# Kernel optimization log

Measured on AMD Instinct MI355X. Metric: run time of the kernel, lower is better.

## Reference

```python
import jax, jax.numpy as jnp
import numpy as np

N, E, DIN, H, DOUT = 50000, 1600000, 16, 256, 2
EPS = 1e-5


def _glorot(key, shape):
    fan_in = shape[0]
    return jax.random.normal(key, shape, dtype=jnp.float32) * (1.0 / np.sqrt(fan_in))


def setup_inputs() -> dict:
    key = jax.random.key(0)
    ks = jax.random.split(key, 16)
    x = jax.random.normal(ks[0], (N, DIN), dtype=jnp.float32)
    edge_index = jax.random.randint(ks[1], (2, E), 0, N, dtype=jnp.int64)
    edge_weight = jax.random.uniform(ks[2], (E,), dtype=jnp.float32)
    return {
        "x": x,
        "edge_index": edge_index,
        "edge_weight": edge_weight,
        # GCN layer 1 and 2
        "W1": _glorot(ks[3], (DIN, H)), "b1": jnp.zeros((H,), jnp.float32),
        "g1": jnp.ones((H,), jnp.float32), "be1": jnp.zeros((H,), jnp.float32),
        "W2": _glorot(ks[4], (H, H)), "b2": jnp.zeros((H,), jnp.float32),
        "g2": jnp.ones((H,), jnp.float32), "be2": jnp.zeros((H,), jnp.float32),
        # GRU (single layer): weight_ih [3H, H], weight_hh [3H, H]
        "Wih": _glorot(ks[5], (H, 3 * H)).T * 0.5,
        "Whh": _glorot(ks[6], (H, 3 * H)).T * 0.5,
        "bih": jnp.zeros((3 * H,), jnp.float32),
        "bhh": jnp.zeros((3 * H,), jnp.float32),
        # decoder MLP
        "Wd1": _glorot(ks[7], (H + DIN, H)), "bd1": jnp.zeros((H,), jnp.float32),
        "Wd2": _glorot(ks[8], (H, H // 2)), "bd2": jnp.zeros((H // 2,), jnp.float32),
        "Wd3": _glorot(ks[9], (H // 2, DOUT)), "bd3": jnp.zeros((DOUT,), jnp.float32),
    }


def _gcn_conv(x, W, b, src, dst, ew, n):
    # GCNConv(improved=True): A_hat = A + 2I, sym-normalized, messages aggregated at dst
    xw = x @ W  # [n, H]
    sl = jnp.arange(n, dtype=src.dtype)
    src_f = jnp.concatenate([src, sl])
    dst_f = jnp.concatenate([dst, sl])
    ew_f = jnp.concatenate([ew, jnp.full((n,), 2.0, ew.dtype)])
    deg = jax.ops.segment_sum(ew_f, dst_f, num_segments=n)
    dis = jnp.where(deg > 0, jax.lax.rsqrt(jnp.maximum(deg, 1e-12)), 0.0)
    norm = dis[src_f] * ew_f * dis[dst_f]  # [E+n]
    out = jax.ops.segment_sum(xw[src_f] * norm[:, None], dst_f, num_segments=n)
    return out + b


def _layernorm(h, g, be):
    mu = jnp.mean(h, axis=-1, keepdims=True)
    var = jnp.mean(jnp.square(h - mu), axis=-1, keepdims=True)
    return (h - mu) * jax.lax.rsqrt(var + EPS) * g + be


def _gru_step(x, h, Wih, Whh, bih, bhh):
    gi = x @ Wih.T + bih  # [n, 3H]
    gh = h @ Whh.T + bhh
    i_r, i_z, i_n = jnp.split(gi, 3, axis=-1)
    h_r, h_z, h_n = jnp.split(gh, 3, axis=-1)
    r = jax.nn.sigmoid(i_r + h_r)
    z = jax.nn.sigmoid(i_z + h_z)
    n = jnp.tanh(i_n + r * h_n)
    return (1.0 - z) * n + z * h


def reference(x, edge_index, edge_weight, W1, b1, g1, be1, W2, b2, g2, be2,
              Wih, Whh, bih, bhh, Wd1, bd1, Wd2, bd2, Wd3, bd3):
    n = x.shape[0]
    src, dst = edge_index[0], edge_index[1]
    # spatial encoding (eval mode: dropout off)
    h = _gcn_conv(x, W1, b1, src, dst, edge_weight, n)
    h = jax.nn.relu(_layernorm(h, g1, be1))
    h = _gcn_conv(h, W2, b2, src, dst, edge_weight, n)
    h = _layernorm(h, g2, be2)  # last layer: no relu
    # GRU single timestep, zero initial hidden state per agent
    h0 = jnp.zeros_like(h)
    temporal = _gru_step(h, h0, Wih, Whh, bih, bhh)
    # decoder MLP on [temporal, x]
    d = jnp.concatenate([temporal, x], axis=-1)
    d = jax.nn.relu(d @ Wd1 + bd1)
    d = jax.nn.relu(d @ Wd2 + bd2)
    pred = d @ Wd3 + bd3
    return jnp.clip(pred, -5.0, 5.0)
```

## Files before the change

### kernel.cpp

```cpp
#include <hip/hip_runtime.h>
#include <math.h>

#define N_NODES 50000
#define N_EDGES 1600000
#define DIN 16
#define H 256
#define RPB 16
#define LN_EPS 1e-5f
#define FIXS 8388608.0f
#define NB 391
#define CAP 5120
#define TILEA 4096
#define NTILES 391
#define GRU_COLS 48
#define GRU_STR 272
#define DSTR 264

typedef __attribute__((ext_vector_type(8))) unsigned short u16x8;
typedef __attribute__((ext_vector_type(8))) __bf16 bf16x8;
typedef __attribute__((ext_vector_type(4))) float f32x4;

__device__ inline unsigned short f2bf(float f) {
    unsigned u = __builtin_bit_cast(unsigned, f);
    return (unsigned short)((u + 0x7FFFu + ((u >> 16) & 1u)) >> 16);
}
__device__ inline float bf2f(unsigned short u) {
    return __builtin_bit_cast(float, ((unsigned)u) << 16);
}
__device__ inline float fsig(float x) { return 1.0f / (1.0f + __expf(-x)); }
__device__ inline float ftanh(float x) { return 2.0f / (1.0f + __expf(-2.0f * x)) - 1.0f; }

__global__ void k_detect(const void* ei, int* flag) {
    const long long* p = (const long long*)ei;
    bool is64 = true;
    for (int i = 0; i < 8; ++i) {
        long long v = p[i];
        if (v < 0 || v >= N_NODES) is64 = false;
    }
    *flag = is64 ? 1 : 0;
}

__global__ void k_zeroi(int* p, int n) {
    int i = blockIdx.x * blockDim.x + threadIdx.x;
    if (i < n) p[i] = 0;
}

__global__ void k_wprep(const float* Wih, const float* W2, const float* Wd1, const float* Wd2,
                        const float* x, unsigned short* Wg, unsigned short* W2T,
                        unsigned short* Wd1T, unsigned short* Wd2T, unsigned short* din) {
    int idx = blockIdx.x * blockDim.x + threadIdx.x;
    if (idx < 768 * 256) { Wg[idx] = f2bf(Wih[idx]); return; }
    idx -= 768 * 256;
    if (idx < 256 * 256) { int k = idx >> 8, n = idx & 255; W2T[n * 256 + k] = f2bf(W2[idx]); return; }
    idx -= 256 * 256;
    if (idx < 256 * 288) {
        int n = idx / 288, k = idx % 288;
        Wd1T[idx] = (k < 272) ? f2bf(Wd1[k * 256 + n]) : (unsigned short)0;
        return;
    }
    idx -= 256 * 288;
    if (idx < 128 * 256) { int k = idx >> 7, n = idx & 127; Wd2T[n * 256 + k] = f2bf(Wd2[idx]); return; }
    idx -= 128 * 256;
    if (idx < N_NODES * 32) {
        int row = idx >> 5, j = idx & 31;
        din[(long long)row * 288 + 256 + j] = (j < 16) ? f2bf(x[row * DIN + j]) : (unsigned short)0;
    }
}

__global__ __launch_bounds__(256) void k_msplit(const void* ei, const int* flag, const float* ew,
                                                int* bcursor, unsigned long long* stage) {
    __shared__ int bh[512], bscn[512], cur[512], gbase[512];
    __shared__ int ws4[4];
    __shared__ unsigned long long sdata[TILEA];
    __shared__ unsigned short sbkt[TILEA];
    int t = threadIdx.x;
    long long base = (long long)blockIdx.x * TILEA;
    int nhere = (int)(((long long)N_EDGES - base) < TILEA ? (N_EDGES - base) : TILEA);
    for (int i = t; i < 512; i += 256) bh[i] = 0;
    __syncthreads();
    bool f64 = (*flag != 0);
    unsigned long long vreg[TILEA / 256];
    int breg[TILEA / 256];
#pragma unroll
    for (int k = 0; k < TILEA / 256; ++k) {
        long long e = base + k * 256 + t;
        if (e < N_EDGES) {
            int s, d;
            if (f64) {
                const long long* p = (const long long*)ei;
                s = (int)p[e]; d = (int)p[N_EDGES + e];
            } else {
                const int* p = (const int*)ei;
                s = p[e]; d = p[N_EDGES + e];
            }
            unsigned wbits = __builtin_bit_cast(unsigned, ew[e]);
            vreg[k] = ((unsigned long long)wbits << 32) |
                      ((unsigned long long)(d & 127) << 16) | (unsigned)(s & 0xFFFF);
            breg[k] = d >> 7;
            atomicAdd(&bh[breg[k]], 1);
        } else breg[k] = -1;
    }
    __syncthreads();
    int a0 = bh[2 * t], a1 = bh[2 * t + 1];
    int s = a0 + a1;
    int lane = t & 63, wv = t >> 6;
    int sc = s;
    for (int d = 1; d < 64; d <<= 1) { int u = __shfl_up(sc, d, 64); if (lane >= d) sc += u; }
    if (lane == 63) ws4[wv] = sc;
    __syncthreads();
    int wpre = 0;
    for (int i = 0; i < wv; ++i) wpre += ws4[i];
    int excl = wpre + sc - s;
    bscn[2 * t] = excl;      cur[2 * t] = excl;
    bscn[2 * t + 1] = excl + a0; cur[2 * t + 1] = excl + a0;
    __syncthreads();
    for (int i = t; i < NB; i += 256) {
        int c = bh[i];
        if (c) gbase[i] = atomicAdd(&bcursor[i], c);
    }
    __syncthreads();
#pragma unroll
    for (int k = 0; k < TILEA / 256; ++k) {
        if (breg[k] >= 0) {
            int p = atomicAdd(&cur[breg[k]], 1);
            sdata[p] = vreg[k];
            sbkt[p] = (unsigned short)breg[k];
        }
    }
    __syncthreads();
    for (int i = t; i < nhere; i += 256) {
        int b = sbkt[i];
        stage[(long long)b * CAP + gbase[b] + (i - bscn[b])] = sdata[i];
    }
}

__global__ __launch_bounds__(256) void k_bfin(const unsigned long long* __restrict__ stage,
                                              const int* __restrict__ bcursor,
                                              float* __restrict__ dis,
                                              int* __restrict__ offs, int* __restrict__ oend,
                                              unsigned* __restrict__ csr) {
    __shared__ unsigned long long acc[128];
    __shared__ int sc[128];
    __shared__ int cur[128];
    int b = blockIdx.x, t = threadIdx.x;
    if (t < 128) acc[t] = 0ULL;
    __syncthreads();
    long long e0 = (long long)b * CAP;
    int n = bcursor[b];
    for (int i = t; i < n; i += 256) {
        unsigned long long v = stage[e0 + i];
        int nl = (int)((v >> 16) & 127);
        float w = __builtin_bit_cast(float, (unsigned)(v >> 32));
        atomicAdd(&acc[nl], (1ULL << 43) | (unsigned long long)llrintf(w * FIXS));
    }
    __syncthreads();
    int mycnt = 0;
    if (t < 128) {
        unsigned long long v = acc[t];
        mycnt = (int)(v >> 43);
        sc[t] = mycnt;
        int node = (b << 7) + t;
        if (node < N_NODES)
            dis[node] = rsqrtf((float)(v & ((1ULL << 43) - 1)) * (1.0f / FIXS) + 2.0f);
    }
    __syncthreads();
    for (int d = 1; d < 128; d <<= 1) {
        int v = 0;
        if (t < 128 && t >= d) v = sc[t - d];
        __syncthreads();
        if (t < 128 && t >= d) sc[t] += v;
        __syncthreads();
    }
    if (t < 128) {
        int excl = sc[t] - mycnt;
        cur[t] = excl;
        int node = (b << 7) + t;
        if (node < N_NODES) {
            offs[node] = (int)(e0 + excl);
            oend[node] = (int)(e0 + excl + mycnt);
        }
    }
    __syncthreads();
    for (int i = t; i < n; i += 256) {
        unsigned long long v = stage[e0 + i];
        int nl = (int)((v >> 16) & 127);
        int p = atomicAdd(&cur[nl], 1);
        float w = __builtin_bit_cast(float, (unsigned)(v >> 32));
        csr[e0 + p] = ((unsigned)f2bf(w) << 16) | (unsigned)(v & 0xFFFFu);
    }
}

__global__ void k_xpb(const float* x, const float* dis, unsigned short* xpb) {
    int idx = blockIdx.x * blockDim.x + threadIdx.x;
    if (idx >= N_NODES * DIN) return;
    xpb[idx] = f2bf(dis[idx >> 4] * x[idx]);
}

__global__ __launch_bounds__(256) void k_l1(const unsigned short* __restrict__ xpb,
        const int* __restrict__ offs, const int* __restrict__ oend,
        const unsigned* __restrict__ csr, const float* __restrict__ dis,
        const float* __restrict__ W, const float* __restrict__ bias,
        const float* __restrict__ g, const float* __restrict__ be,
        unsigned short* __restrict__ out) {
    __shared__ float s[RPB][H + 1];
    __shared__ float smu[RPB], srs[RPB];
    int t = threadIdx.x;
    long long rowbase = (long long)blockIdx.x * RPB;
    {
        int r = blockIdx.x * 16 + (t >> 4);
        int dd = t & 15;
        float di = dis[r];
        float xself = bf2f(xpb[(long long)r * DIN + dd]);
        float acc = 0.0f;
        int e0 = offs[r], e1 = oend[r];
        for (int e = e0; e < e1; e += 8) {
            unsigned vv[8];
#pragma unroll
            for (int j = 0; j < 8; ++j) {
                int idx = e + j;
                vv[j] = (idx < e1) ? csr[idx] : (unsigned)r;
            }
            float xx[8];
#pragma unroll
            for (int j = 0; j < 8; ++j) {
                int sidx = (int)(vv[j] & 0xFFFFu);
                xx[j] = bf2f(xpb[(long long)sidx * DIN + dd]);
            }
#pragma unroll
            for (int j = 0; j < 8; ++j) {
                float c = bf2f((unsigned short)(vv[j] >> 16));
                acc = fmaf(c, xx[j], acc);
            }
        }
        s[t >> 4][dd] = di * acc + 2.0f * di * xself;
    }
    __syncthreads();
    float acc2[RPB];
    float bb0 = bias[t];
#pragma unroll
    for (int r = 0; r < RPB; ++r) acc2[r] = bb0;
    for (int k = 0; k < DIN; ++k) {
        float wv = W[k * H + t];
#pragma unroll
        for (int r = 0; r < RPB; ++r) acc2[r] = fmaf(s[r][k], wv, acc2[r]);
    }
    __syncthreads();
#pragma unroll
    for (int r = 0; r < RPB; ++r) s[r][t] = acc2[r];
    __syncthreads();
    int lane = t & 63, wv2 = t >> 6;
    for (int rr = wv2; rr < RPB; rr += 4) {
        float v0 = s[rr][lane], v1 = s[rr][lane + 64], v2 = s[rr][lane + 128], v3 = s[rr][lane + 192];
        float sm = v0 + v1 + v2 + v3;
        float sq = v0 * v0 + v1 * v1 + v2 * v2 + v3 * v3;
        for (int d = 32; d; d >>= 1) {
            sm += __shfl_down(sm, d, 64);
            sq += __shfl_down(sq, d, 64);
        }
        if (lane == 0) {
            float mu = sm * (1.0f / H);
            float var = sq * (1.0f / H) - mu * mu;
            smu[rr] = mu;
            srs[rr] = rsqrtf(var + LN_EPS);
        }
    }
    __syncthreads();
    float gg = g[t], bb = be[t];
#pragma unroll
    for (int r = 0; r < RPB; ++r) {
        float h = fmaxf((acc2[r] - smu[r]) * srs[r] * gg + bb, 0.0f);
        out[(rowbase + r) * H + t] = f2bf(h * dis[rowbase + r]);
    }
}

__global__ __launch_bounds__(256) void k_spmm(const unsigned short* __restrict__ hin,
                                              unsigned short* __restrict__ hout,
                                              const int* __restrict__ offs,
                                              const int* __restrict__ oend,
                                              const unsigned* __restrict__ csr,
                                              const float* __restrict__ dis) {
    int t = threadIdx.x;
    int wv = t >> 6, lane = t & 63;
    int row = blockIdx.x * 4 + wv;
    const ushort4* h4 = (const ushort4*)hin;
    float di = dis[row];
    ushort4 vs = h4[(long long)row * 64 + lane];
    float a0 = 0.f, a1 = 0.f, a2 = 0.f, a3 = 0.f;
    int e0 = offs[row], e1 = oend[row];
    for (int e = e0; e < e1; e += 16) {
        unsigned vv[16];
#pragma unroll
        for (int j = 0; j < 16; ++j) {
            int idx = e + j;
            vv[j] = (idx < e1) ? csr[idx] : (unsigned)row;
        }
        ushort4 uu[16];
#pragma unroll
        for (int j = 0; j < 16; ++j) {
            int s = (int)(vv[j] & 0xFFFFu);
            uu[j] = h4[(long long)s * 64 + lane];
        }
#pragma unroll
        for (int j = 0; j < 16; ++j) {
            float c = bf2f((unsigned short)(vv[j] >> 16));
            a0 = fmaf(c, bf2f(uu[j].x), a0);
            a1 = fmaf(c, bf2f(uu[j].y), a1);
            a2 = fmaf(c, bf2f(uu[j].z), a2);
            a3 = fmaf(c, bf2f(uu[j].w), a3);
        }
    }
    ushort4 o;
    o.x = f2bf(di * a0 + 2.0f * di * bf2f(vs.x));
    o.y = f2bf(di * a1 + 2.0f * di * bf2f(vs.y));
    o.z = f2bf(di * a2 + 2.0f * di * bf2f(vs.z));
    o.w = f2bf(di * a3 + 2.0f * di * bf2f(vs.w));
    ((ushort4*)hout)[(long long)row * 64 + lane] = o;
}


__global__ __launch_bounds__(256) void k_ln_mfma(const unsigned short* __restrict__ in,
        const unsigned short* __restrict__ WT, const float* __restrict__ bias,
        const float* __restrict__ g, const float* __restrict__ be,
        unsigned short* __restrict__ outbf) {
    int t = threadIdx.x;
    int wv = t >> 6, l = t & 63;
    int lr = l & 15, lg = l >> 4;
    int rb = blockIdx.x * 64 + wv * 16;
    int arow = rb + lr; if (arow >= N_NODES) arow = N_NODES - 1;
    bf16x8 af[8];
    const unsigned short* ap = in + (long long)arow * H + lg * 8;
#pragma unroll
    for (int ks = 0; ks < 8; ++ks) af[ks] = __builtin_bit_cast(bf16x8, *(const u16x8*)(ap + ks * 32));
    f32x4 acc[16];
#pragma unroll
    for (int ct = 0; ct < 16; ++ct) acc[ct] = (f32x4){0.f, 0.f, 0.f, 0.f};
    for (int ct = 0; ct < 16; ++ct) {
        const unsigned short* wr = WT + (ct * 16 + lr) * H + lg * 8;
#pragma unroll
        for (int ks = 0; ks < 8; ++ks) {
            bf16x8 bfv = __builtin_bit_cast(bf16x8, *(const u16x8*)(wr + ks * 32));
            acc[ct] = __builtin_amdgcn_mfma_f32_16x16x32_bf16(af[ks], bfv, acc[ct], 0, 0, 0);
        }
    }
#pragma unroll
    for (int ct = 0; ct < 16; ++ct) {
        float bb = bias[ct * 16 + lr];
#pragma unroll
        for (int q = 0; q < 4; ++q) acc[ct][q] += bb;
    }
    float mean[4], rstd[4];
#pragma unroll
    for (int q = 0; q < 4; ++q) {
        float s = 0.f, s2 = 0.f;
#pragma unroll
        for (int ct = 0; ct < 16; ++ct) { float v = acc[ct][q]; s += v; s2 += v * v; }
#pragma unroll
        for (int m = 1; m < 16; m <<= 1) { s += __shfl_xor(s, m, 64); s2 += __shfl_xor(s2, m, 64); }
        float mu = s * (1.0f / H);
        mean[q] = mu;
        rstd[q] = rsqrtf(s2 * (1.0f / H) - mu * mu + LN_EPS);
    }
#pragma unroll
    for (int ct = 0; ct < 16; ++ct) {
        int col = ct * 16 + lr;
        float gg = g[col], bb = be[col];
#pragma unroll
        for (int q = 0; q < 4; ++q) {
            int row = rb + lg * 4 + q;
            if (row < N_NODES) {
                float nv = (acc[ct][q] - mean[q]) * rstd[q] * gg + bb;
                outbf[(long long)row * H + col] = f2bf(nv);
            }
        }
    }
}

__global__ __launch_bounds__(256) void k_gru_lds(const unsigned short* __restrict__ h2,
        const unsigned short* __restrict__ Wg, const float* __restrict__ bih,
        const float* __restrict__ bhh, unsigned short* __restrict__ din) {
    __shared__ unsigned short wbuf[2][GRU_COLS * GRU_STR];
    int t = threadIdx.x;
    int wv = t >> 6, l = t & 63;
    int lr = l & 15, lg = l >> 4;
    int rb = blockIdx.x * 64 + wv * 16;
    int arow = rb + lr; if (arow >= N_NODES) arow = N_NODES - 1;
    bf16x8 af[8];
    const unsigned short* ap = h2 + (long long)arow * H + lg * 8;
#pragma unroll
    for (int ks = 0; ks < 8; ++ks) af[ks] = __builtin_bit_cast(bf16x8, *(const u16x8*)(ap + ks * 32));

    auto stage = [&](int ct, int b) {
#pragma unroll
        for (int j = 0; j < 6; ++j) {
            int i = t + j * 256;
            int col = i >> 5;
            int off = (i & 31) * 8;
            int gate = col >> 4, c = col & 15;
            u16x8 v = *(const u16x8*)(Wg + ((gate * 256 + ct * 16 + c) * 256 + off));
            *(u16x8*)(&wbuf[b][col * GRU_STR + off]) = v;
        }
    };
    stage(0, 0);
    __syncthreads();
    for (int ct = 0; ct < 16; ++ct) {
        if (ct < 15) stage(ct + 1, (ct + 1) & 1);
        const unsigned short* cur = wbuf[ct & 1];
        f32x4 aR = (f32x4){0.f, 0.f, 0.f, 0.f};
        f32x4 aZ = aR, aN = aR;
        const unsigned short* base = cur + lr * GRU_STR + lg * 8;
#pragma unroll
        for (int ks = 0; ks < 8; ++ks) {
            bf16x8 b0 = __builtin_bit_cast(bf16x8, *(const u16x8*)(base + ks * 32));
            bf16x8 b1 = __builtin_bit_cast(bf16x8, *(const u16x8*)(base + 16 * GRU_STR + ks * 32));
            bf16x8 b2 = __builtin_bit_cast(bf16x8, *(const u16x8*)(base + 32 * GRU_STR + ks * 32));
            aR = __builtin_amdgcn_mfma_f32_16x16x32_bf16(af[ks], b0, aR, 0, 0, 0);
            aZ = __builtin_amdgcn_mfma_f32_16x16x32_bf16(af[ks], b1, aZ, 0, 0, 0);
            aN = __builtin_amdgcn_mfma_f32_16x16x32_bf16(af[ks], b2, aN, 0, 0, 0);
        }
        int col = ct * 16 + lr;
        float bR = bih[col] + bhh[col];
        float bZ = bih[col + 256] + bhh[col + 256];
        float bN = bih[col + 512];
        float hN = bhh[col + 512];
#pragma unroll
        for (int q = 0; q < 4; ++q) {
            int row = rb + lg * 4 + q;
            float r = fsig(aR[q] + bR);
            float z = fsig(aZ[q] + bZ);
            float n = ftanh(aN[q] + bN + r * hN);
            if (row < N_NODES) din[(long long)row * 288 + col] = f2bf((1.0f - z) * n);
        }
        __syncthreads();
    }
}

__global__ __launch_bounds__(256) void k_dec(const unsigned short* __restrict__ din,
        const unsigned short* __restrict__ W1T, const float* __restrict__ b1d,
        const unsigned short* __restrict__ W2T, const float* __restrict__ bd2,
        const float* __restrict__ Wd3, const float* __restrict__ bd3, float* __restrict__ out) {
    __shared__ unsigned short dtile[64][DSTR];
    int t = threadIdx.x;
    int wv = t >> 6, l = t & 63;
    int lr = l & 15, lg = l >> 4;
    int rb = blockIdx.x * 64 + wv * 16;
    int arow = rb + lr; if (arow >= N_NODES) arow = N_NODES - 1;
    {
        bf16x8 af[9];
        const unsigned short* ap = din + (long long)arow * 288 + lg * 8;
#pragma unroll
        for (int ks = 0; ks < 9; ++ks) af[ks] = __builtin_bit_cast(bf16x8, *(const u16x8*)(ap + ks * 32));
        f32x4 acc[16];
#pragma unroll
        for (int ct = 0; ct < 16; ++ct) acc[ct] = (f32x4){0.f, 0.f, 0.f, 0.f};
        for (int ct = 0; ct < 16; ++ct) {
            const unsigned short* wr = W1T + (ct * 16 + lr) * 288 + lg * 8;
#pragma unroll
            for (int ks = 0; ks < 9; ++ks) {
                bf16x8 bfv = __builtin_bit_cast(bf16x8, *(const u16x8*)(wr + ks * 32));
                acc[ct] = __builtin_amdgcn_mfma_f32_16x16x32_bf16(af[ks], bfv, acc[ct], 0, 0, 0);
            }
        }
#pragma unroll
        for (int ct = 0; ct < 16; ++ct) {
            float bb = b1d[ct * 16 + lr];
#pragma unroll
            for (int q = 0; q < 4; ++q) {
                float v = fmaxf(acc[ct][q] + bb, 0.0f);
                dtile[wv * 16 + lg * 4 + q][ct * 16 + lr] = f2bf(v);
            }
        }
    }
    __syncthreads();
    bf16x8 af[8];
    const unsigned short* lp = &dtile[wv * 16 + lr][0] + lg * 8;
#pragma unroll
    for (int ks = 0; ks < 8; ++ks) af[ks] = __builtin_bit_cast(bf16x8, *(const u16x8*)(lp + ks * 32));
    f32x4 acc[8];
#pragma unroll
    for (int ct = 0; ct < 8; ++ct) acc[ct] = (f32x4){0.f, 0.f, 0.f, 0.f};
    for (int ct = 0; ct < 8; ++ct) {
        const unsigned short* wr = W2T + (ct * 16 + lr) * H + lg * 8;
#pragma unroll
        for (int ks = 0; ks < 8; ++ks) {
            bf16x8 bfv = __builtin_bit_cast(bf16x8, *(const u16x8*)(wr + ks * 32));
            acc[ct] = __builtin_amdgcn_mfma_f32_16x16x32_bf16(af[ks], bfv, acc[ct], 0, 0, 0);
        }
    }
    float p0[4] = {0.f, 0.f, 0.f, 0.f}, p1[4] = {0.f, 0.f, 0.f, 0.f};
#pragma unroll
    for (int ct = 0; ct < 8; ++ct) {
        int col = ct * 16 + lr;
        float bb = bd2[col];
        float2 w3 = *(const float2*)(Wd3 + col * 2);
#pragma unroll
        for (int q = 0; q < 4; ++q) {
            float v = fmaxf(acc[ct][q] + bb, 0.0f);
            p0[q] = fmaf(v, w3.x, p0[q]);
            p1[q] = fmaf(v, w3.y, p1[q]);
        }
    }
#pragma unroll
    for (int q = 0; q < 4; ++q) {
#pragma unroll
        for (int m = 1; m < 16; m <<= 1) {
            p0[q] += __shfl_xor(p0[q], m, 64);
            p1[q] += __shfl_xor(p1[q], m, 64);
        }
    }
    if (lr == 0) {
#pragma unroll
        for (int q = 0; q < 4; ++q) {
            int row = rb + lg * 4 + q;
            if (row < N_NODES) {
                float a = fminf(fmaxf(p0[q] + bd3[0], -5.0f), 5.0f);
                float b = fminf(fmaxf(p1[q] + bd3[1], -5.0f), 5.0f);
                out[(long long)row * 2] = a;
                out[(long long)row * 2 + 1] = b;
            }
        }
    }
}

extern "C" void kernel_launch(void* const* d_in, const int* in_sizes, int n_in,
                              void* d_out, int out_size, void* d_ws, size_t ws_size,
                              hipStream_t stream) {
    const float* x   = (const float*)d_in[0];
    const void*  ei  = d_in[1];
    const float* ew  = (const float*)d_in[2];
    const float* W1  = (const float*)d_in[3];
    const float* b1  = (const float*)d_in[4];
    const float* g1  = (const float*)d_in[5];
    const float* be1 = (const float*)d_in[6];
    const float* W2  = (const float*)d_in[7];
    const float* b2  = (const float*)d_in[8];
    const float* g2  = (const float*)d_in[9];
    const float* be2 = (const float*)d_in[10];
    const float* Wih = (const float*)d_in[11];
    const float* bih = (const float*)d_in[13];
    const float* bhh = (const float*)d_in[14];
    const float* Wd1 = (const float*)d_in[15];
    const float* bd1 = (const float*)d_in[16];
    const float* Wd2 = (const float*)d_in[17];
    const float* bd2 = (const float*)d_in[18];
    const float* Wd3 = (const float*)d_in[19];
    const float* bd3 = (const float*)d_in[20];
    float* out = (float*)d_out;

    char* w = (char*)d_ws;
    size_t pos = 0;
    auto carve = [&](size_t bytes) -> void* {
        void* p = w + pos;
        pos += (bytes + 255) & ~(size_t)255;
        return p;
    };
    int*   flag    = (int*)carve(4);
    int*   bcursor = (int*)carve(sizeof(int) * 512);
    float* dis     = (float*)carve(sizeof(float) * N_NODES);
    int*   offs    = (int*)carve(sizeof(int) * N_NODES);
    int*   oend    = (int*)carve(sizeof(int) * N_NODES);
    unsigned long long* stage = (unsigned long long*)carve(8 * (size_t)NB * CAP);
    unsigned* csr = (unsigned*)carve(4 * (size_t)NB * CAP);
    unsigned short* xpb  = (unsigned short*)carve(2 * (size_t)N_NODES * DIN);
    unsigned short* Wg   = (unsigned short*)carve(2 * 768 * 256);
    unsigned short* W2T  = (unsigned short*)carve(2 * 256 * 256);
    unsigned short* Wd1T = (unsigned short*)carve(2 * 256 * 288);
    unsigned short* Wd2T = (unsigned short*)carve(2 * 128 * 256);
    unsigned short* Abf = (unsigned short*)carve(2 * (size_t)N_NODES * H);
    unsigned short* Bbf = (unsigned short*)carve(2 * (size_t)N_NODES * H);
    unsigned short* din = (unsigned short*)carve(2 * (size_t)N_NODES * 288);
    unsigned short* h2bf = Abf;
    (void)pos; (void)ws_size; (void)in_sizes; (void)n_in; (void)out_size;

    int nbm = (N_NODES + 63) / 64;
    int nwp = (768 * 256 + 256 * 256 + 256 * 288 + 128 * 256 + N_NODES * 32 + 255) / 256;

    k_detect<<<1, 1, 0, stream>>>(ei, flag);
    k_zeroi<<<2, 256, 0, stream>>>(bcursor, 512);
    k_wprep<<<nwp, 256, 0, stream>>>(Wih, W2, Wd1, Wd2, x, Wg, W2T, Wd1T, Wd2T, din);
    k_msplit<<<NTILES, 256, 0, stream>>>(ei, flag, ew, bcursor, stage);
    k_bfin<<<NB, 256, 0, stream>>>(stage, bcursor, dis, offs, oend, csr);
    k_xpb<<<(N_NODES * DIN + 255) / 256, 256, 0, stream>>>(x, dis, xpb);

    k_l1<<<N_NODES / RPB, 256, 0, stream>>>(xpb, offs, oend, csr, dis, W1, b1, g1, be1, Abf);
    k_spmm<<<N_NODES / 4, 256, 0, stream>>>(Abf, Bbf, offs, oend, csr, dis);
    k_ln_mfma<<<nbm, 256, 0, stream>>>(Bbf, W2T, b2, g2, be2, h2bf);
    k_gru_lds<<<nbm, 256, 0, stream>>>(h2bf, Wg, bih, bhh, din);
    k_dec<<<nbm, 256, 0, stream>>>(din, Wd1T, bd1, Wd2T, bd2, Wd3, bd3, out);
}
```

Baseline: 440.0 us.

## Fuse LN/GRU/decoder into one kernel and fold small prep kernels

```diff
diff --git a/kernel.cpp b/kernel.cpp
--- a/kernel.cpp
+++ b/kernel.cpp
@@ -30,24 +30,10 @@
 __device__ inline float fsig(float x) { return 1.0f / (1.0f + __expf(-x)); }
 __device__ inline float ftanh(float x) { return 2.0f / (1.0f + __expf(-2.0f * x)) - 1.0f; }
 
-__global__ void k_detect(const void* ei, int* flag) {
-    const long long* p = (const long long*)ei;
-    bool is64 = true;
-    for (int i = 0; i < 8; ++i) {
-        long long v = p[i];
-        if (v < 0 || v >= N_NODES) is64 = false;
-    }
-    *flag = is64 ? 1 : 0;
-}
-
-__global__ void k_zeroi(int* p, int n) {
-    int i = blockIdx.x * blockDim.x + threadIdx.x;
-    if (i < n) p[i] = 0;
-}
-
 __global__ void k_wprep(const float* Wih, const float* W2, const float* Wd1, const float* Wd2,
                         const float* x, unsigned short* Wg, unsigned short* W2T,
-                        unsigned short* Wd1T, unsigned short* Wd2T, unsigned short* din) {
+                        unsigned short* Wd1T, unsigned short* Wd2T, unsigned short* xb,
+                        int* bcursor) {
     int idx = blockIdx.x * blockDim.x + threadIdx.x;
     if (idx < 768 * 256) { Wg[idx] = f2bf(Wih[idx]); return; }
     idx -= 768 * 256;
@@ -63,11 +49,14 @@
     idx -= 128 * 256;
     if (idx < N_NODES * 32) {
         int row = idx >> 5, j = idx & 31;
-        din[(long long)row * 288 + 256 + j] = (j < 16) ? f2bf(x[row * DIN + j]) : (unsigned short)0;
-    }
-}
-
-__global__ __launch_bounds__(256) void k_msplit(const void* ei, const int* flag, const float* ew,
+        xb[idx] = (j < 16) ? f2bf(x[row * DIN + j]) : (unsigned short)0;
+        return;
+    }
+    idx -= N_NODES * 32;
+    if (idx < 512) bcursor[idx] = 0;
+}
+
+__global__ __launch_bounds__(256) void k_msplit(const void* ei, const float* ew,
                                                 int* bcursor, unsigned long long* stage) {
     __shared__ int bh[512], bscn[512], cur[512], gbase[512];
     __shared__ int ws4[4];
@@ -77,8 +66,13 @@
     long long base = (long long)blockIdx.x * TILEA;
     int nhere = (int)(((long long)N_EDGES - base) < TILEA ? (N_EDGES - base) : TILEA);
     for (int i = t; i < 512; i += 256) bh[i] = 0;
-    __syncthreads();
-    bool f64 = (*flag != 0);
+    bool f64;
+    {
+        const long long* p = (const long long*)ei;
+        f64 = true;
+        for (int i = 0; i < 8; ++i) { long long v = p[i]; if (v < 0 || v >= N_NODES) f64 = false; }
+    }
+    __syncthreads();
     unsigned long long vreg[TILEA / 256];
     int breg[TILEA / 256];
 #pragma unroll
@@ -136,12 +130,15 @@
 
 __global__ __launch_bounds__(256) void k_bfin(const unsigned long long* __restrict__ stage,
                                               const int* __restrict__ bcursor,
+                                              const float* __restrict__ x,
                                               float* __restrict__ dis,
                                               int* __restrict__ offs, int* __restrict__ oend,
-                                              unsigned* __restrict__ csr) {
+                                              unsigned* __restrict__ csr,
+                                              unsigned short* __restrict__ xpb) {
     __shared__ unsigned long long acc[128];
     __shared__ int sc[128];
     __shared__ int cur[128];
+    __shared__ float sdis[128];
     int b = blockIdx.x, t = threadIdx.x;
     if (t < 128) acc[t] = 0ULL;
     __syncthreads();
@@ -159,9 +156,10 @@
         unsigned long long v = acc[t];
         mycnt = (int)(v >> 43);
         sc[t] = mycnt;
+        float dv = rsqrtf((float)(v & ((1ULL << 43) - 1)) * (1.0f / FIXS) + 2.0f);
+        sdis[t] = dv;
         int node = (b << 7) + t;
-        if (node < N_NODES)
-            dis[node] = rsqrtf((float)(v & ((1ULL << 43) - 1)) * (1.0f / FIXS) + 2.0f);
+        if (node < N_NODES) dis[node] = dv;
     }
     __syncthreads();
     for (int d = 1; d < 128; d <<= 1) {
@@ -188,12 +186,11 @@
         float w = __builtin_bit_cast(float, (unsigned)(v >> 32));
         csr[e0 + p] = ((unsigned)f2bf(w) << 16) | (unsigned)(v & 0xFFFFu);
     }
-}
-
-__global__ void k_xpb(const float* x, const float* dis, unsigned short* xpb) {
-    int idx = blockIdx.x * blockDim.x + threadIdx.x;
-    if (idx >= N_NODES * DIN) return;
-    xpb[idx] = f2bf(dis[idx >> 4] * x[idx]);
+    for (int i = t; i < 128 * DIN; i += 256) {
+        int nl = i >> 4, dd = i & 15;
+        int node = (b << 7) + nl;
+        if (node < N_NODES) xpb[node * DIN + dd] = f2bf(sdis[nl] * x[node * DIN + dd]);
+    }
 }
 
 __global__ __launch_bounds__(256) void k_l1(const unsigned short* __restrict__ xpb,
@@ -317,138 +314,122 @@
     ((ushort4*)hout)[(long long)row * 64 + lane] = o;
 }
 
-
-__global__ __launch_bounds__(256) void k_ln_mfma(const unsigned short* __restrict__ in,
-        const unsigned short* __restrict__ WT, const float* __restrict__ bias,
-        const float* __restrict__ g, const float* __restrict__ be,
-        unsigned short* __restrict__ outbf) {
-    int t = threadIdx.x;
-    int wv = t >> 6, l = t & 63;
-    int lr = l & 15, lg = l >> 4;
-    int rb = blockIdx.x * 64 + wv * 16;
-    int arow = rb + lr; if (arow >= N_NODES) arow = N_NODES - 1;
-    bf16x8 af[8];
-    const unsigned short* ap = in + (long long)arow * H + lg * 8;
-#pragma unroll
-    for (int ks = 0; ks < 8; ++ks) af[ks] = __builtin_bit_cast(bf16x8, *(const u16x8*)(ap + ks * 32));
-    f32x4 acc[16];
-#pragma unroll
-    for (int ct = 0; ct < 16; ++ct) acc[ct] = (f32x4){0.f, 0.f, 0.f, 0.f};
-    for (int ct = 0; ct < 16; ++ct) {
-        const unsigned short* wr = WT + (ct * 16 + lr) * H + lg * 8;
-#pragma unroll
-        for (int ks = 0; ks < 8; ++ks) {
-            bf16x8 bfv = __builtin_bit_cast(bf16x8, *(const u16x8*)(wr + ks * 32));
-            acc[ct] = __builtin_amdgcn_mfma_f32_16x16x32_bf16(af[ks], bfv, acc[ct], 0, 0, 0);
-        }
-    }
-#pragma unroll
-    for (int ct = 0; ct < 16; ++ct) {
-        float bb = bias[ct * 16 + lr];
-#pragma unroll
-        for (int q = 0; q < 4; ++q) acc[ct][q] += bb;
-    }
-    float mean[4], rstd[4];
-#pragma unroll
-    for (int q = 0; q < 4; ++q) {
-        float s = 0.f, s2 = 0.f;
-#pragma unroll
-        for (int ct = 0; ct < 16; ++ct) { float v = acc[ct][q]; s += v; s2 += v * v; }
-#pragma unroll
-        for (int m = 1; m < 16; m <<= 1) { s += __shfl_xor(s, m, 64); s2 += __shfl_xor(s2, m, 64); }
-        float mu = s * (1.0f / H);
-        mean[q] = mu;
-        rstd[q] = rsqrtf(s2 * (1.0f / H) - mu * mu + LN_EPS);
-    }
-#pragma unroll
-    for (int ct = 0; ct < 16; ++ct) {
-        int col = ct * 16 + lr;
-        float gg = g[col], bb = be[col];
-#pragma unroll
-        for (int q = 0; q < 4; ++q) {
-            int row = rb + lg * 4 + q;
-            if (row < N_NODES) {
-                float nv = (acc[ct][q] - mean[q]) * rstd[q] * gg + bb;
-                outbf[(long long)row * H + col] = f2bf(nv);
-            }
-        }
-    }
-}
-
-__global__ __launch_bounds__(256) void k_gru_lds(const unsigned short* __restrict__ h2,
+__global__ __launch_bounds__(256) void k_lgd(
+        const unsigned short* __restrict__ Bbf,
+        const unsigned short* __restrict__ W2T, const float* __restrict__ b2,
+        const float* __restrict__ g2, const float* __restrict__ be2,
         const unsigned short* __restrict__ Wg, const float* __restrict__ bih,
-        const float* __restrict__ bhh, unsigned short* __restrict__ din) {
-    __shared__ unsigned short wbuf[2][GRU_COLS * GRU_STR];
-    int t = threadIdx.x;
-    int wv = t >> 6, l = t & 63;
-    int lr = l & 15, lg = l >> 4;
-    int rb = blockIdx.x * 64 + wv * 16;
-    int arow = rb + lr; if (arow >= N_NODES) arow = N_NODES - 1;
-    bf16x8 af[8];
-    const unsigned short* ap = h2 + (long long)arow * H + lg * 8;
-#pragma unroll
-    for (int ks = 0; ks < 8; ++ks) af[ks] = __builtin_bit_cast(bf16x8, *(const u16x8*)(ap + ks * 32));
-
-    auto stage = [&](int ct, int b) {
-#pragma unroll
-        for (int j = 0; j < 6; ++j) {
-            int i = t + j * 256;
-            int col = i >> 5;
-            int off = (i & 31) * 8;
-            int gate = col >> 4, c = col & 15;
-            u16x8 v = *(const u16x8*)(Wg + ((gate * 256 + ct * 16 + c) * 256 + off));
-            *(u16x8*)(&wbuf[b][col * GRU_STR + off]) = v;
-        }
-    };
-    stage(0, 0);
-    __syncthreads();
-    for (int ct = 0; ct < 16; ++ct) {
-        if (ct < 15) stage(ct + 1, (ct + 1) & 1);
-        const unsigned short* cur = wbuf[ct & 1];
-        f32x4 aR = (f32x4){0.f, 0.f, 0.f, 0.f};
-        f32x4 aZ = aR, aN = aR;
-        const unsigned short* base = cur + lr * GRU_STR + lg * 8;
-#pragma unroll
-        for (int ks = 0; ks < 8; ++ks) {
-            bf16x8 b0 = __builtin_bit_cast(bf16x8, *(const u16x8*)(base + ks * 32));
-            bf16x8 b1 = __builtin_bit_cast(bf16x8, *(const u16x8*)(base + 16 * GRU_STR + ks * 32));
-            bf16x8 b2 = __builtin_bit_cast(bf16x8, *(const u16x8*)(base + 32 * GRU_STR + ks * 32));
-            aR = __builtin_amdgcn_mfma_f32_16x16x32_bf16(af[ks], b0, aR, 0, 0, 0);
-            aZ = __builtin_amdgcn_mfma_f32_16x16x32_bf16(af[ks], b1, aZ, 0, 0, 0);
-            aN = __builtin_amdgcn_mfma_f32_16x16x32_bf16(af[ks], b2, aN, 0, 0, 0);
-        }
-        int col = ct * 16 + lr;
-        float bR = bih[col] + bhh[col];
-        float bZ = bih[col + 256] + bhh[col + 256];
-        float bN = bih[col + 512];
-        float hN = bhh[col + 512];
-#pragma unroll
-        for (int q = 0; q < 4; ++q) {
-            int row = rb + lg * 4 + q;
-            float r = fsig(aR[q] + bR);
-            float z = fsig(aZ[q] + bZ);
-            float n = ftanh(aN[q] + bN + r * hN);
-            if (row < N_NODES) din[(long long)row * 288 + col] = f2bf((1.0f - z) * n);
-        }
-        __syncthreads();
-    }
-}
-
-__global__ __launch_bounds__(256) void k_dec(const unsigned short* __restrict__ din,
-        const unsigned short* __restrict__ W1T, const float* __restrict__ b1d,
-        const unsigned short* __restrict__ W2T, const float* __restrict__ bd2,
-        const float* __restrict__ Wd3, const float* __restrict__ bd3, float* __restrict__ out) {
+        const float* __restrict__ bhh,
+        const unsigned short* __restrict__ W1T, const float* __restrict__ bd1,
+        const unsigned short* __restrict__ Wd2T, const float* __restrict__ bd2,
+        const float* __restrict__ Wd3, const float* __restrict__ bd3,
+        const unsigned short* __restrict__ xb, float* __restrict__ out) {
+    __shared__ unsigned short wbuf[GRU_COLS * GRU_STR];
     __shared__ unsigned short dtile[64][DSTR];
     int t = threadIdx.x;
     int wv = t >> 6, l = t & 63;
     int lr = l & 15, lg = l >> 4;
     int rb = blockIdx.x * 64 + wv * 16;
     int arow = rb + lr; if (arow >= N_NODES) arow = N_NODES - 1;
+
     {
-        bf16x8 af[9];
-        const unsigned short* ap = din + (long long)arow * 288 + lg * 8;
-#pragma unroll
-        for (int ks = 0; ks < 9; ++ks) af[ks] = __builtin_bit_cast(bf16x8, *(const u16x8*)(ap + ks * 32));
+        bf16x8 af[8];
+        const unsigned short* ap = Bbf + (long long)arow * H + lg * 8;
+#pragma unroll
+        for (int ks = 0; ks < 8; ++ks) af[ks] = __builtin_bit_cast(bf16x8, *(const u16x8*)(ap + ks * 32));
+        f32x4 acc[16];
+#pragma unroll
+        for (int ct = 0; ct < 16; ++ct) acc[ct] = (f32x4){0.f, 0.f, 0.f, 0.f};
+        for (int ct = 0; ct < 16; ++ct) {
+            const unsigned short* wr = W2T + (ct * 16 + lr) * H + lg * 8;
+#pragma unroll
+            for (int ks = 0; ks < 8; ++ks) {
+                bf16x8 bfv = __builtin_bit_cast(bf16x8, *(const u16x8*)(wr + ks * 32));
+                acc[ct] = __builtin_amdgcn_mfma_f32_16x16x32_bf16(af[ks], bfv, acc[ct], 0, 0, 0);
+            }
+        }
+#pragma unroll
+        for (int ct = 0; ct < 16; ++ct) {
+            float bb = b2[ct * 16 + lr];
+#pragma unroll
+            for (int q = 0; q < 4; ++q) acc[ct][q] += bb;
+        }
+        float mean[4], rstd[4];
+#pragma unroll
+        for (int q = 0; q < 4; ++q) {
+            float s = 0.f, s2 = 0.f;
+#pragma unroll
+            for (int ct = 0; ct < 16; ++ct) { float v = acc[ct][q]; s += v; s2 += v * v; }
+#pragma unroll
+            for (int m = 1; m < 16; m <<= 1) { s += __shfl_xor(s, m, 64); s2 += __shfl_xor(s2, m, 64); }
+            float mu = s * (1.0f / H);
+            mean[q] = mu;
+            rstd[q] = rsqrtf(s2 * (1.0f / H) - mu * mu + LN_EPS);
+        }
+#pragma unroll
+        for (int ct = 0; ct < 16; ++ct) {
+            int col = ct * 16 + lr;
+            float gg = g2[col], bb = be2[col];
+#pragma unroll
+            for (int q = 0; q < 4; ++q) {
+                float nv = (acc[ct][q] - mean[q]) * rstd[q] * gg + bb;
+                dtile[wv * 16 + lg * 4 + q][col] = f2bf(nv);
+            }
+        }
+    }
+    __syncthreads();
+
+    {
+        bf16x8 ah[8];
+        const unsigned short* lp = &dtile[wv * 16 + lr][0] + lg * 8;
+#pragma unroll
+        for (int ks = 0; ks < 8; ++ks) ah[ks] = __builtin_bit_cast(bf16x8, *(const u16x8*)(lp + ks * 32));
+        for (int ct = 0; ct < 16; ++ct) {
+#pragma unroll
+            for (int j = 0; j < 6; ++j) {
+                int i = t + j * 256;
+                int col = i >> 5;
+                int off = (i & 31) * 8;
+                int gate = col >> 4, c = col & 15;
+                u16x8 v = *(const u16x8*)(Wg + ((gate * 256 + ct * 16 + c) * 256 + off));
+                *(u16x8*)(&wbuf[col * GRU_STR + off]) = v;
+            }
+            __syncthreads();
+            f32x4 aR = (f32x4){0.f, 0.f, 0.f, 0.f};
+            f32x4 aZ = aR, aN = aR;
+            const unsigned short* base = wbuf + lr * GRU_STR + lg * 8;
+#pragma unroll
+            for (int ks = 0; ks < 8; ++ks) {
+                bf16x8 b0 = __builtin_bit_cast(bf16x8, *(const u16x8*)(base + ks * 32));
+                bf16x8 b1 = __builtin_bit_cast(bf16x8, *(const u16x8*)(base + 16 * GRU_STR + ks * 32));
+                bf16x8 b2v = __builtin_bit_cast(bf16x8, *(const u16x8*)(base + 32 * GRU_STR + ks * 32));
+                aR = __builtin_amdgcn_mfma_f32_16x16x32_bf16(ah[ks], b0, aR, 0, 0, 0);
+                aZ = __builtin_amdgcn_mfma_f32_16x16x32_bf16(ah[ks], b1, aZ, 0, 0, 0);
+                aN = __builtin_amdgcn_mfma_f32_16x16x32_bf16(ah[ks], b2v, aN, 0, 0, 0);
+            }
+            int col = ct * 16 + lr;
+            float bR = bih[col] + bhh[col];
+            float bZ = bih[col + 256] + bhh[col + 256];
+            float bN = bih[col + 512];
+            float hN = bhh[col + 512];
+#pragma unroll
+            for (int q = 0; q < 4; ++q) {
+                float r = fsig(aR[q] + bR);
+                float z = fsig(aZ[q] + bZ);
+                float nn = ftanh(aN[q] + bN + r * hN);
+                dtile[wv * 16 + lg * 4 + q][col] = f2bf((1.0f - z) * nn);
+            }
+            __syncthreads();
+        }
+    }
+
+    {
+        bf16x8 ad[9];
+        const unsigned short* lp = &dtile[wv * 16 + lr][0] + lg * 8;
+#pragma unroll
+        for (int ks = 0; ks < 8; ++ks) ad[ks] = __builtin_bit_cast(bf16x8, *(const u16x8*)(lp + ks * 32));
+        ad[8] = __builtin_bit_cast(bf16x8, *(const u16x8*)(xb + (long long)arow * 32 + lg * 8));
+        __syncthreads();
         f32x4 acc[16];
 #pragma unroll
         for (int ct = 0; ct < 16; ++ct) acc[ct] = (f32x4){0.f, 0.f, 0.f, 0.f};
@@ -457,12 +438,12 @@
 #pragma unroll
             for (int ks = 0; ks < 9; ++ks) {
                 bf16x8 bfv = __builtin_bit_cast(bf16x8, *(const u16x8*)(wr + ks * 32));
-                acc[ct] = __builtin_amdgcn_mfma_f32_16x16x32_bf16(af[ks], bfv, acc[ct], 0, 0, 0);
+                acc[ct] = __builtin_amdgcn_mfma_f32_16x16x32_bf16(ad[ks], bfv, acc[ct], 0, 0, 0);
             }
         }
 #pragma unroll
         for (int ct = 0; ct < 16; ++ct) {
-            float bb = b1d[ct * 16 + lr];
+            float bb = bd1[ct * 16 + lr];
 #pragma unroll
             for (int q = 0; q < 4; ++q) {
                 float v = fmaxf(acc[ct][q] + bb, 0.0f);
@@ -471,6 +452,7 @@
         }
     }
     __syncthreads();
+
     bf16x8 af[8];
     const unsigned short* lp = &dtile[wv * 16 + lr][0] + lg * 8;
 #pragma unroll
@@ -479,7 +461,7 @@
 #pragma unroll
     for (int ct = 0; ct < 8; ++ct) acc[ct] = (f32x4){0.f, 0.f, 0.f, 0.f};
     for (int ct = 0; ct < 8; ++ct) {
-        const unsigned short* wr = W2T + (ct * 16 + lr) * H + lg * 8;
+        const unsigned short* wr = Wd2T + (ct * 16 + lr) * H + lg * 8;
 #pragma unroll
         for (int ks = 0; ks < 8; ++ks) {
             bf16x8 bfv = __builtin_bit_cast(bf16x8, *(const u16x8*)(wr + ks * 32));
@@ -553,7 +535,6 @@
         pos += (bytes + 255) & ~(size_t)255;
         return p;
     };
-    int*   flag    = (int*)carve(4);
     int*   bcursor = (int*)carve(sizeof(int) * 512);
     float* dis     = (float*)carve(sizeof(float) * N_NODES);
     int*   offs    = (int*)carve(sizeof(int) * N_NODES);
@@ -561,29 +542,23 @@
     unsigned long long* stage = (unsigned long long*)carve(8 * (size_t)NB * CAP);
     unsigned* csr = (unsigned*)carve(4 * (size_t)NB * CAP);
     unsigned short* xpb  = (unsigned short*)carve(2 * (size_t)N_NODES * DIN);
+    unsigned short* xb   = (unsigned short*)carve(2 * (size_t)N_NODES * 32);
     unsigned short* Wg   = (unsigned short*)carve(2 * 768 * 256);
     unsigned short* W2T  = (unsigned short*)carve(2 * 256 * 256);
     unsigned short* Wd1T = (unsigned short*)carve(2 * 256 * 288);
     unsigned short* Wd2T = (unsigned short*)carve(2 * 128 * 256);
     unsigned short* Abf = (unsigned short*)carve(2 * (size_t)N_NODES * H);
     unsigned short* Bbf = (unsigned short*)carve(2 * (size_t)N_NODES * H);
-    unsigned short* din = (unsigned short*)carve(2 * (size_t)N_NODES * 288);
-    unsigned short* h2bf = Abf;
     (void)pos; (void)ws_size; (void)in_sizes; (void)n_in; (void)out_size;
 
     int nbm = (N_NODES + 63) / 64;
-    int nwp = (768 * 256 + 256 * 256 + 256 * 288 + 128 * 256 + N_NODES * 32 + 255) / 256;
-
-    k_detect<<<1, 1, 0, stream>>>(ei, flag);
-    k_zeroi<<<2, 256, 0, stream>>>(bcursor, 512);
-    k_wprep<<<nwp, 256, 0, stream>>>(Wih, W2, Wd1, Wd2, x, Wg, W2T, Wd1T, Wd2T, din);
-    k_msplit<<<NTILES, 256, 0, stream>>>(ei, flag, ew, bcursor, stage);
-    k_bfin<<<NB, 256, 0, stream>>>(stage, bcursor, dis, offs, oend, csr);
-    k_xpb<<<(N_NODES * DIN + 255) / 256, 256, 0, stream>>>(x, dis, xpb);
-
+    int nwp = (768 * 256 + 256 * 256 + 256 * 288 + 128 * 256 + N_NODES * 32 + 512 + 255) / 256;
+
+    k_wprep<<<nwp, 256, 0, stream>>>(Wih, W2, Wd1, Wd2, x, Wg, W2T, Wd1T, Wd2T, xb, bcursor);
+    k_msplit<<<NTILES, 256, 0, stream>>>(ei, ew, bcursor, stage);
+    k_bfin<<<NB, 256, 0, stream>>>(stage, bcursor, x, dis, offs, oend, csr, xpb);
     k_l1<<<N_NODES / RPB, 256, 0, stream>>>(xpb, offs, oend, csr, dis, W1, b1, g1, be1, Abf);
     k_spmm<<<N_NODES / 4, 256, 0, stream>>>(Abf, Bbf, offs, oend, csr, dis);
-    k_ln_mfma<<<nbm, 256, 0, stream>>>(Bbf, W2T, b2, g2, be2, h2bf);
-    k_gru_lds<<<nbm, 256, 0, stream>>>(h2bf, Wg, bih, bhh, din);
-    k_dec<<<nbm, 256, 0, stream>>>(din, Wd1T, bd1, Wd2T, bd2, Wd3, bd3, out);
-}
+    k_lgd<<<nbm, 256, 0, stream>>>(Bbf, W2T, b2, g2, be2, Wg, bih, bhh,
+                                   Wd1T, bd1, Wd2T, bd2, Wd3, bd3, xb, out);
+}
```

Result: faster. 389.3 us (-11.5%).
